# Optimization experiments

Measured on AMD Instinct MI355X. Metric: run time of the kernel, lower is better.

The kernel has to match this reference:

```python
import jax, jax.numpy as jnp
import numpy as np

B, S_IN, IN_DIM, HID, H, W = 256, 2, 2304, 512, 7, 7
SCALE = 1.0 / float(np.sqrt(HID))


def setup_inputs() -> dict:
    key = jax.random.key(0)
    ks = jax.random.split(key, 13)
    w = lambda k, shp: (jax.random.normal(k, shp, dtype=jnp.float32) * 0.02)
    return {
        "status": jax.random.normal(ks[0], (B, S_IN), dtype=jnp.float32),
        "rois": jax.random.uniform(ks[1], (B, 5), dtype=jnp.float32),
        "bbox_feat": jax.random.normal(ks[2], (B, IN_DIM, 1, H, W), dtype=jnp.float32),
        "conv_w": w(ks[3], (HID, IN_DIM, 3, 3)),
        "q1_w": w(ks[4], (HID, S_IN + 4)),
        "k1_w": w(ks[5], (HID, HID)),
        "k2_w": w(ks[6], (HID, HID)),
        "v1_w": w(ks[7], (HID, HID)),
        "v2_w": w(ks[8], (HID, HID)),
        "proj1_w": w(ks[9], (HID, HID)),
        "proj1_b": jnp.zeros((HID,), dtype=jnp.float32),
        "proj2_w": w(ks[10], (HID, HID)),
        "proj2_b": jnp.zeros((HID,), dtype=jnp.float32),
    }


def reference(status, rois, bbox_feat, conv_w, q1_w, k1_w, k2_w, v1_w, v2_w,
              proj1_w, proj1_b, proj2_w, proj2_b):
    x = bbox_feat[:, :, 0]  # squeeze(2) -> [B, IN_DIM, H, W]
    feat = jax.lax.conv_general_dilated(
        x, conv_w, window_strides=(1, 1), padding="SAME",
        dimension_numbers=("NCHW", "OIHW", "NCHW"))  # [B, HID, H, W]
    b, c, h, w_ = feat.shape
    hw = h * w_
    feat_seq = feat.reshape(b, c, hw).transpose(0, 2, 1)  # [B, HW, HID]
    st = jnp.concatenate([status, rois[:, 1:]], axis=1)   # [B, status_dim]
    # query is identical at every spatial position (status broadcast over HW),
    # so attention rows are identical -> compute once per batch element.
    q = st @ q1_w.T  # [B, HID] (forward uses q1 for both branches; q2 is dead code)

    def branch(k_w, v_w, p_w, p_b):
        k = feat_seq @ k_w.T                      # [B, HW, HID]
        v = feat_seq @ v_w.T                      # [B, HW, HID]
        logits = jnp.einsum("bd,bnd->bn", q, k) * SCALE
        att = jax.nn.softmax(logits, axis=-1)     # [B, HW]
        virt = jnp.einsum("bn,bnd->bd", att, v)   # [B, HID]
        virt = virt @ p_w.T + p_b                 # proj (dropout = identity in eval)
        out = feat_seq + virt[:, None, :]         # residual, broadcast over HW
        return out.transpose(0, 2, 1).reshape(b, c, h, w_)[:, :, None]  # [B,HID,1,H,W]

    out1 = branch(k1_w, v1_w, proj1_w, proj1_b)
    out2 = branch(k2_w, v2_w, proj2_w, proj2_b)
    return (out1, out2)
```

## Files before the change

### kernel.cpp

```cpp
#include <hip/hip_runtime.h>
#include <hip/hip_bf16.h>
#include <stdint.h>

#define CIN   2304
#define HID_  512
#define NP    12544
#define OUT1  6422528

typedef float  f32x4 __attribute__((ext_vector_type(4)));
typedef short  s16x8 __attribute__((ext_vector_type(8)));

__device__ __forceinline__ uint16_t f2bf(float f) {
  uint32_t x = __builtin_bit_cast(uint32_t, f);
  return (uint16_t)((x + 0x7FFFu + ((x >> 16) & 1u)) >> 16);
}
__device__ __forceinline__ float bf2f(uint16_t u) {
  return __builtin_bit_cast(float, ((uint32_t)u) << 16);
}
__device__ __forceinline__ void gload16(const void* g, void* l) {
  __builtin_amdgcn_global_load_lds((const __attribute__((address_space(1))) void*)g,
                                   (__attribute__((address_space(3))) void*)l, 16, 0, 0);
}

__global__ __launch_bounds__(256) void prep_all_k(const float* __restrict__ xs,
    const float* __restrict__ cw, const float* __restrict__ q1w,
    const float* __restrict__ k1w, const float* __restrict__ k2w,
    const float* __restrict__ v1w, const float* __restrict__ v2w,
    const float* __restrict__ p1w, const float* __restrict__ p2w,
    uint16_t* __restrict__ xT, uint16_t* __restrict__ Wt,
    float* __restrict__ A, float* __restrict__ PVt) {
  __shared__ __align__(16) char sm[18448];
  const int tid = threadIdx.x;
  const int bi = blockIdx.x;
  if (bi < 9216) {
    float* t = (float*)sm;
    const int cg = bi % 36, b = bi / 36;
    const int c0 = cg * 64;
    const float4* src = (const float4*)(xs + ((size_t)b * CIN + c0) * 49);
    for (int i = tid; i < 784; i += 256) ((float4*)t)[i] = src[i];
    __syncthreads();
    for (int j = tid; j < 392; j += 256) {
      const int s = j >> 3, cq = j & 7;
      union { uint16_t us[8]; uint4 v; } pk;
#pragma unroll
      for (int q = 0; q < 8; ++q) pk.us[q] = f2bf(t[(cq * 8 + q) * 49 + s]);
      *(uint4*)(xT + ((size_t)(b * 49 + s) * CIN + c0 + cq * 8)) = pk.v;
    }
  } else if (bi < 18432) {
    float* t = (float*)sm;
    const int rest = bi - 9216;
    const int cg = rest % 18, o = rest / 18;
    const int c0 = cg * 128;
    const float* src = cw + ((size_t)o * CIN + c0) * 9;
    for (int i = tid; i < 1152; i += 256) t[i] = src[i];
    __syncthreads();
    if (tid < 144) {
      const int tp = tid >> 4, c8 = tid & 15;
      union { uint16_t us[8]; uint4 v; } pk;
#pragma unroll
      for (int q = 0; q < 8; ++q) pk.us[q] = f2bf(t[(c8 * 8 + q) * 9 + tp]);
      *(uint4*)(Wt + ((size_t)(tp * HID_ + o) * CIN + c0 + c8 * 8)) = pk.v;
    }
  } else if (bi < 18448) {
    float* q1s = (float*)sm;
    float (*red)[6][64] = (float(*)[6][64])(sm + 12288);
    const int rest = bi - 18432;
    const int e0 = (rest & 7) * 64, ib = rest >> 3;
    const int g = tid >> 6, l = tid & 63;
    for (int i = tid; i < 3072; i += 256) q1s[i] = q1w[i];
    __syncthreads();
    const float* kw = (ib ? k2w : k1w) + e0 + l;
    float acc[6] = {};
#pragma unroll 4
    for (int d = g * 128; d < (g + 1) * 128; ++d) {
      const float kv = kw[(size_t)d * 512];
#pragma unroll
      for (int j = 0; j < 6; ++j) acc[j] += q1s[d * 6 + j] * kv;
    }
#pragma unroll
    for (int j = 0; j < 6; ++j) red[g][j][l] = acc[j];
    __syncthreads();
    for (int i2 = tid; i2 < 384; i2 += 256) {
      const int j = i2 >> 6, l2 = i2 & 63;
      A[(ib * 6 + j) * 512 + e0 + l2] =
          red[0][j][l2] + red[1][j][l2] + red[2][j][l2] + red[3][j][l2];
    }
  } else {
    float* Av  = (float*)sm;
    float* Bpt = (float*)(sm + 8192);
    const int rest = bi - 18448;
    const int ibz = rest >> 6, r2 = rest & 63;
    const int d0 = (r2 & 7) * 64, e0 = (r2 >> 3) * 64;
    const float* vw = ibz ? v2w : v1w;
    const float* pw = ibz ? p2w : p1w;
    const int tx = tid & 15, ty = tid >> 4;
    float acc[4][4] = {};
    for (int m0 = 0; m0 < 512; m0 += 32) {
      __syncthreads();
      for (int i = tid; i < 2048; i += 256) {
        Av[i] = vw[(size_t)(m0 + (i >> 6)) * 512 + e0 + (i & 63)];
        Bpt[(i & 31) * 68 + (i >> 5)] = pw[(size_t)(d0 + (i >> 5)) * 512 + m0 + (i & 31)];
      }
      __syncthreads();
#pragma unroll 4
      for (int mm = 0; mm < 32; ++mm) {
        const float4 bv = *(const float4*)&Bpt[mm * 68 + tx * 4];
        const float4 av = *(const float4*)&Av[mm * 64 + ty * 4];
        const float a0[4] = {av.x, av.y, av.z, av.w};
        const float b0[4] = {bv.x, bv.y, bv.z, bv.w};
#pragma unroll
        for (int ee = 0; ee < 4; ++ee)
#pragma unroll
          for (int dd = 0; dd < 4; ++dd) acc[ee][dd] += a0[ee] * b0[dd];
      }
    }
#pragma unroll
    for (int ee = 0; ee < 4; ++ee) {
      float4 r; r.x = acc[ee][0]; r.y = acc[ee][1]; r.z = acc[ee][2]; r.w = acc[ee][3];
      *(float4*)&PVt[ibz * 262144 + (size_t)(e0 + ty * 4 + ee) * 512 + d0 + tx * 4] = r;
    }
  }
}

#define LDSX1  11520
#define LDSW   23040
#define LDSZ   72192
__global__ __launch_bounds__(256) void conv_k(const uint16_t* __restrict__ xT,
    const uint16_t* __restrict__ Wt, uint16_t* __restrict__ feat0,
    uint16_t* __restrict__ feat1) {
  __shared__ __align__(16) char lds[72208];
  const int tid = threadIdx.x;
  const int wid = tid >> 6;
  const int lane = tid & 63;
  const int g16 = (lane >> 4) << 4;
  const int l15 = lane & 15;
  const int ww = wid & 1, wm = wid >> 1;

  const int idx = blockIdx.x;
  const int sp = idx & 1;
  const int bn = (idx >> 1) & 3;
  const int bm = idx >> 3;
  const int n0 = bm * 128;
  const int o0 = bn * 128;
  const int c0 = sp * 36;

  const int rb0 = (wm * 64 + l15) * 80 + 640 + g16;
  int maskb[4];
#pragma unroll
  for (int m = 0; m < 4; ++m) {
    const int p = (n0 + wm * 64 + m * 16 + l15) % 49;
    const int y = p / 7, xx = p - y * 7;
    int mb = 0;
#pragma unroll
    for (int t = 0; t < 9; ++t) {
      const int yy = y + t / 3 - 1, xc = xx + t % 3 - 1;
      if (yy >= 0 && yy < 7 && xc >= 0 && xc < 7) mb |= 1 << t;
    }
    maskb[m] = mb;
  }

  const int wb0 = ww * 4096 + l15 * 64 + (g16 ^ (((l15 >> 1) & 3) << 4));

  const char* WtB = (const char*)Wt;
  const char* xTB = (const char*)xT;
  int wsrc[6];
#pragma unroll
  for (int q = 0; q < 6; ++q) {
    const int slot = q * 256 + tid;
    const int tsub = slot >> 9;
    const int ss = slot & 511;
    const int row = ss >> 2, unit = ss & 3;
    const int lu = unit ^ ((row >> 1) & 3);
    wsrc[q] = tsub * 2359296 + (o0 + row) * 4608 + lu * 16;
  }
  int xsrc[3], xv[3];
#pragma unroll
  for (int k = 0; k < 3; ++k) {
    const int slot = k * 256 + tid;
    xv[k] = slot < 720;
    const int row = slot / 5;
    int unit = slot - row * 5; if (unit > 3) unit = 3;
    int nr = n0 - 8 + row;
    nr = nr < 0 ? 0 : (nr > NP - 1 ? NP - 1 : nr);
    xsrc[k] = nr * (CIN * 2) + unit * 16;
  }

  if (tid < 4) *(int*)(lds + LDSZ + tid * 4) = 0;
  __syncthreads();

#define XSTAGE(CC1) { \
    const char* xb_ = xTB + (size_t)(CC1) * 64; \
    char* xd_ = lds + ((CC1) & 1) * LDSX1 + wid * 1024; \
    if (xv[0]) gload16(xb_ + xsrc[0], xd_); \
    if (xv[1]) gload16(xb_ + xsrc[1], xd_ + 4096); \
    if (xv[2]) gload16(xb_ + xsrc[2], xd_ + 8192); }

#define WSTAGE(T0, CC, WB) { \
    const char* wb_ = WtB + (size_t)(T0) * 2359296 + (size_t)(CC) * 64; \
    char* wd_ = lds + LDSW + (WB) * 24576 + wid * 1024; \
    gload16(wb_ + wsrc[0], wd_); \
    gload16(wb_ + wsrc[1], wd_ + 4096); \
    gload16(wb_ + wsrc[2], wd_ + 8192); \
    gload16(wb_ + wsrc[3], wd_ + 12288); \
    gload16(wb_ + wsrc[4], wd_ + 16384); \
    gload16(wb_ + wsrc[5], wd_ + 20480); }

#define TAP(TT, WB, XSEL) \
    { const int wof_ = LDSW + (WB) * 24576 + ((TT) % 3) * 8192; \
      s16x8 bfr_[4]; \
      _Pragma("unroll") \
      for (int n_ = 0; n_ < 4; ++n_) \
        bfr_[n_] = *(const s16x8*)(lds + wof_ + wb0 + n_ * 1024); \
      __builtin_amdgcn_s_setprio(1); \
      _Pragma("unroll") \
      for (int m_ = 0; m_ < 4; ++m_) { \
        const int off_ = m_ * 1280 + (((TT) / 3 - 1) * 7 + ((TT) % 3 - 1)) * 80; \
        const int ab_ = ((maskb[m_] >> (TT)) & 1) ? (rb0 + (XSEL)) : (LDSZ - off_); \
        const s16x8 af_ = *(const s16x8*)(lds + ab_ + off_); \
        _Pragma("unroll") \
        for (int n_ = 0; n_ < 4; ++n_) \
          acc[m_][n_] = __builtin_amdgcn_mfma_f32_16x16x32_bf16(af_, bfr_[n_], acc[m_][n_], 0, 0, 0); \
      } \
      __builtin_amdgcn_s_setprio(0); }

#define SYNC \
    asm volatile("s_waitcnt vmcnt(0)" ::: "memory"); \
    __builtin_amdgcn_s_barrier(); \
    __builtin_amdgcn_sched_barrier(0);

  XSTAGE(c0);
  WSTAGE(0, c0, 0);
  f32x4 acc[4][4] = {};
  SYNC

#pragma unroll 1
  for (int i = 0; i < 18; ++i) {
    const int ccA = c0 + 2 * i, ccB = ccA + 1;
    WSTAGE(3, ccA, 1); XSTAGE(ccB);
    TAP(0, 0, 0) TAP(1, 0, 0) TAP(2, 0, 0)
    SYNC
    WSTAGE(6, ccA, 0);
    TAP(3, 1, 0) TAP(4, 1, 0) TAP(5, 1, 0)
    SYNC
    WSTAGE(0, ccB, 1);
    TAP(6, 0, 0) TAP(7, 0, 0) TAP(8, 0, 0)
    SYNC
    WSTAGE(3, ccB, 0);
    if (i < 17) { XSTAGE(ccB + 1); }
    TAP(0, 1, LDSX1) TAP(1, 1, LDSX1) TAP(2, 1, LDSX1)
    SYNC
    WSTAGE(6, ccB, 1);
    TAP(3, 0, LDSX1) TAP(4, 0, LDSX1) TAP(5, 0, LDSX1)
    SYNC
    if (i < 17) { WSTAGE(0, ccB + 1, 0); }
    TAP(6, 1, LDSX1) TAP(7, 1, LDSX1) TAP(8, 1, LDSX1)
    SYNC
  }
#undef TAP
#undef WSTAGE
#undef XSTAGE
#undef SYNC

  uint16_t* fb = (sp ? feat1 : feat0) +
                 ((size_t)(n0 + wm * 64)) * HID_ + o0 + ww * 64;
  const int g4 = (lane >> 4) * 4;
#pragma unroll
  for (int m = 0; m < 4; ++m)
#pragma unroll
    for (int n = 0; n < 4; ++n)
#pragma unroll
      for (int r = 0; r < 4; ++r)
        fb[(m * 16 + g4 + r) * HID_ + n * 16 + l15] = f2bf(acc[m][n][r]);
}

#define FLP 520
__global__ __launch_bounds__(256) void att_k(const uint16_t* __restrict__ feat0,
    const uint16_t* __restrict__ feat1,
    const float* __restrict__ status, const float* __restrict__ rois,
    const float* __restrict__ A, const float* __restrict__ PVt,
    const float* __restrict__ pb1, const float* __restrict__ pb2,
    float* __restrict__ out) {
  __shared__ uint16_t fl[49 * FLP];
  __shared__ float qk[512];
  __shared__ float attv[64];
  __shared__ float fbar[512];
  __shared__ float v2[512];
  __shared__ float part[256];
  const int tid = threadIdx.x;
  const int b = blockIdx.x >> 1, ib = blockIdx.x & 1;

  const uint4* s0 = (const uint4*)(feat0 + (size_t)b * 25088);
  const uint4* s1 = (const uint4*)(feat1 + (size_t)b * 25088);
  for (int i = tid; i < 3136; i += 256) {
    const int n = i >> 6, e8 = (i & 63) << 3;
    union { uint16_t us[8]; uint4 v; } a, c, r;
    a.v = s0[i]; c.v = s1[i];
#pragma unroll
    for (int q = 0; q < 8; ++q) r.us[q] = f2bf(bf2f(a.us[q]) + bf2f(c.us[q]));
    *(uint4*)&fl[n * FLP + e8] = r.v;
  }
  float st6[6];
  st6[0] = status[b * 2]; st6[1] = status[b * 2 + 1];
#pragma unroll
  for (int j = 0; j < 4; ++j) st6[2 + j] = rois[b * 5 + 1 + j];
  for (int e = tid; e < 512; e += 256) {
    const float* Ai = A + ib * 3072;
    float s = 0.f;
#pragma unroll
    for (int j = 0; j < 6; ++j) s += st6[j] * Ai[j * 512 + e];
    qk[e] = s;
  }
  __syncthreads();

  if (tid < 196) {
    const int n = tid >> 2;
    const int e0 = (tid & 3) * 128;
    float s = 0.f;
    for (int e = e0; e < e0 + 128; ++e) s += bf2f(fl[n * FLP + e]) * qk[e];
    part[tid] = s;
  }
  __syncthreads();
  if (tid < 64) {
    float l = -1e30f;
    if (tid < 49)
      l = 0.044194173824159216f *
          (part[tid * 4] + part[tid * 4 + 1] + part[tid * 4 + 2] + part[tid * 4 + 3]);
    float mx = l;
#pragma unroll
    for (int o = 32; o > 0; o >>= 1) mx = fmaxf(mx, __shfl_xor(mx, o, 64));
    const float ex = (tid < 49) ? __expf(l - mx) : 0.f;
    float sm = ex;
#pragma unroll
    for (int o = 32; o > 0; o >>= 1) sm += __shfl_xor(sm, o, 64);
    if (tid < 49) attv[tid] = ex / sm;
  }
  __syncthreads();
  for (int e = tid; e < 512; e += 256) {
    float s = 0.f;
#pragma unroll 7
    for (int n = 0; n < 49; ++n) s += attv[n] * bf2f(fl[n * FLP + e]);
    fbar[e] = s;
  }
  __syncthreads();
  for (int d = tid; d < 512; d += 256) {
    const float* P = PVt + ib * 262144 + d;
    float s = (ib ? pb2 : pb1)[d];
#pragma unroll 8
    for (int e = 0; e < 512; ++e) s += P[(size_t)e * 512] * fbar[e];
    v2[d] = s;
  }
  __syncthreads();
  float* ob = out + (size_t)ib * OUT1 + (size_t)b * 25088;
  for (int w = tid; w < 25088; w += 256) {
    const int c = w / 49, p = w - c * 49;
    ob[w] = bf2f(fl[p * FLP + c]) + v2[c];
  }
}

extern "C" void kernel_launch(void* const* d_in, const int* in_sizes, int n_in,
                              void* d_out, int out_size, void* d_ws, size_t ws_size,
                              hipStream_t stream) {
  const float* status = (const float*)d_in[0];
  const float* rois   = (const float*)d_in[1];
  const float* bbox   = (const float*)d_in[2];
  const float* convw  = (const float*)d_in[3];
  const float* q1w    = (const float*)d_in[4];
  const float* k1w    = (const float*)d_in[5];
  const float* k2w    = (const float*)d_in[6];
  const float* v1w    = (const float*)d_in[7];
  const float* v2w    = (const float*)d_in[8];
  const float* p1w    = (const float*)d_in[9];
  const float* p1b    = (const float*)d_in[10];
  const float* p2w    = (const float*)d_in[11];
  const float* p2b    = (const float*)d_in[12];
  float* out = (float*)d_out;
  char* ws = (char*)d_ws;
  uint16_t* xT    = (uint16_t*)(ws);
  uint16_t* Wt    = (uint16_t*)(ws + 57802752);
  uint16_t* feat0 = (uint16_t*)(ws + 79036416);
  uint16_t* feat1 = (uint16_t*)(ws + 91881472);
  float*    PVt   = (float*)(ws + 104726528);
  float*    A     = (float*)(ws + 106823680);
  if (ws_size < 106848256) return;

  hipLaunchKernelGGL(prep_all_k, dim3(18576), dim3(256), 0, stream,
                     bbox, convw, q1w, k1w, k2w, v1w, v2w, p1w, p2w, xT, Wt, A, PVt);
  hipLaunchKernelGGL(conv_k, dim3(784), dim3(256), 0, stream, xT, Wt, feat0, feat1);
  hipLaunchKernelGGL(att_k,  dim3(512), dim3(256), 0, stream, feat0, feat1,
                     status, rois, A, PVt, p1b, p2b, out);
}
```

Baseline: 466.9 us.

## Stage conv weights one tap at a time to shrink LDS and raise occupancy

The conv kernel now double-buffers weights per single 3x3 tap (8 KB per buffer) instead of per group of three taps (24 KB). This shrinks LDS from about 72 KB to about 39 KB and adds a launch-bounds hint of 4 blocks per CU, so more workgroups can be resident at once. In exchange there are three times as many barriers and waitcnt points per channel chunk, with less MFMA work between syncs to hide each load.

```diff
diff --git a/kernel.cpp b/kernel.cpp
--- a/kernel.cpp
+++ b/kernel.cpp
@@ -124,11 +124,11 @@
 
 #define LDSX1  11520
 #define LDSW   23040
-#define LDSZ   72192
-__global__ __launch_bounds__(256) void conv_k(const uint16_t* __restrict__ xT,
+#define LDSZ   39424
+__global__ __launch_bounds__(256, 4) void conv_k(const uint16_t* __restrict__ xT,
     const uint16_t* __restrict__ Wt, uint16_t* __restrict__ feat0,
     uint16_t* __restrict__ feat1) {
-  __shared__ __align__(16) char lds[72208];
+  __shared__ __align__(16) char lds[39440];
   const int tid = threadIdx.x;
   const int wid = tid >> 6;
   const int lane = tid & 63;
@@ -163,15 +163,13 @@
 
   const char* WtB = (const char*)Wt;
   const char* xTB = (const char*)xT;
-  int wsrc[6];
-#pragma unroll
-  for (int q = 0; q < 6; ++q) {
-    const int slot = q * 256 + tid;
-    const int tsub = slot >> 9;
-    const int ss = slot & 511;
-    const int row = ss >> 2, unit = ss & 3;
+  int wsrc[2];
+#pragma unroll
+  for (int j = 0; j < 2; ++j) {
+    const int slot = j * 256 + tid;
+    const int row = slot >> 2, unit = slot & 3;
     const int lu = unit ^ ((row >> 1) & 3);
-    wsrc[q] = tsub * 2359296 + (o0 + row) * 4608 + lu * 16;
+    wsrc[j] = (o0 + row) * 4608 + lu * 16;
   }
   int xsrc[3], xv[3];
 #pragma unroll
@@ -195,22 +193,17 @@
     if (xv[1]) gload16(xb_ + xsrc[1], xd_ + 4096); \
     if (xv[2]) gload16(xb_ + xsrc[2], xd_ + 8192); }
 
-#define WSTAGE(T0, CC, WB) { \
-    const char* wb_ = WtB + (size_t)(T0) * 2359296 + (size_t)(CC) * 64; \
-    char* wd_ = lds + LDSW + (WB) * 24576 + wid * 1024; \
+#define WSTAGE(T, CC, WB) { \
+    const char* wb_ = WtB + (size_t)(T) * 2359296 + (size_t)(CC) * 64; \
+    char* wd_ = lds + LDSW + (WB) * 8192 + wid * 1024; \
     gload16(wb_ + wsrc[0], wd_); \
-    gload16(wb_ + wsrc[1], wd_ + 4096); \
-    gload16(wb_ + wsrc[2], wd_ + 8192); \
-    gload16(wb_ + wsrc[3], wd_ + 12288); \
-    gload16(wb_ + wsrc[4], wd_ + 16384); \
-    gload16(wb_ + wsrc[5], wd_ + 20480); }
+    gload16(wb_ + wsrc[1], wd_ + 4096); }
 
 #define TAP(TT, WB, XSEL) \
-    { const int wof_ = LDSW + (WB) * 24576 + ((TT) % 3) * 8192; \
-      s16x8 bfr_[4]; \
+    { s16x8 bfr_[4]; \
       _Pragma("unroll") \
       for (int n_ = 0; n_ < 4; ++n_) \
-        bfr_[n_] = *(const s16x8*)(lds + wof_ + wb0 + n_ * 1024); \
+        bfr_[n_] = *(const s16x8*)(lds + LDSW + (WB) * 8192 + wb0 + n_ * 1024); \
       __builtin_amdgcn_s_setprio(1); \
       _Pragma("unroll") \
       for (int m_ = 0; m_ < 4; ++m_) { \
@@ -236,24 +229,27 @@
 #pragma unroll 1
   for (int i = 0; i < 18; ++i) {
     const int ccA = c0 + 2 * i, ccB = ccA + 1;
-    WSTAGE(3, ccA, 1); XSTAGE(ccB);
-    TAP(0, 0, 0) TAP(1, 0, 0) TAP(2, 0, 0)
-    SYNC
-    WSTAGE(6, ccA, 0);
-    TAP(3, 1, 0) TAP(4, 1, 0) TAP(5, 1, 0)
-    SYNC
-    WSTAGE(0, ccB, 1);
-    TAP(6, 0, 0) TAP(7, 0, 0) TAP(8, 0, 0)
-    SYNC
-    WSTAGE(3, ccB, 0);
+    XSTAGE(ccB);
+    WSTAGE(1, ccA, 1) TAP(0, 0, 0) SYNC
+    WSTAGE(2, ccA, 0) TAP(1, 1, 0) SYNC
+    WSTAGE(3, ccA, 1) TAP(2, 0, 0) SYNC
+    WSTAGE(4, ccA, 0) TAP(3, 1, 0) SYNC
+    WSTAGE(5, ccA, 1) TAP(4, 0, 0) SYNC
+    WSTAGE(6, ccA, 0) TAP(5, 1, 0) SYNC
+    WSTAGE(7, ccA, 1) TAP(6, 0, 0) SYNC
+    WSTAGE(8, ccA, 0) TAP(7, 1, 0) SYNC
+    WSTAGE(0, ccB, 1) TAP(8, 0, 0) SYNC
     if (i < 17) { XSTAGE(ccB + 1); }
-    TAP(0, 1, LDSX1) TAP(1, 1, LDSX1) TAP(2, 1, LDSX1)
-    SYNC
-    WSTAGE(6, ccB, 1);
-    TAP(3, 0, LDSX1) TAP(4, 0, LDSX1) TAP(5, 0, LDSX1)
-    SYNC
-    if (i < 17) { WSTAGE(0, ccB + 1, 0); }
-    TAP(6, 1, LDSX1) TAP(7, 1, LDSX1) TAP(8, 1, LDSX1)
+    WSTAGE(1, ccB, 0) TAP(0, 1, LDSX1) SYNC
+    WSTAGE(2, ccB, 1) TAP(1, 0, LDSX1) SYNC
+    WSTAGE(3, ccB, 0) TAP(2, 1, LDSX1) SYNC
+    WSTAGE(4, ccB, 1) TAP(3, 0, LDSX1) SYNC
+    WSTAGE(5, ccB, 0) TAP(4, 1, LDSX1) SYNC
+    WSTAGE(6, ccB, 1) TAP(5, 0, LDSX1) SYNC
+    WSTAGE(7, ccB, 0) TAP(6, 1, LDSX1) SYNC
+    WSTAGE(8, ccB, 1) TAP(7, 0, LDSX1) SYNC
+    if (i < 17) { WSTAGE(0, ccB + 1, 0) }
+    TAP(8, 1, LDSX1)
     SYNC
   }
 #undef TAP
```

Measured after the change: 725.0 us. 55.3% more time.
